# Kernel tuning notes

Hardware: AMD Instinct MI355X
Metric: run time of the kernel (lower is better)

## Reference

```python
import jax, jax.numpy as jnp
import numpy as np

B, S, IN, H, NH = 64, 512, 512, 1024, 4
HD = H // NH
A, HID = 18, 1024
EPS = 1e-5


def _ln(x, w, eps=EPS):
    mu = jnp.mean(x, axis=-1, keepdims=True)
    var = jnp.mean((x - mu) ** 2, axis=-1, keepdims=True)
    return (x - mu) * jax.lax.rsqrt(var + eps) * w


def setup_inputs() -> dict:
    key = jax.random.key(0)
    ks = jax.random.split(key, 12)
    g = lambda k, shape, s: jax.random.normal(k, shape, jnp.float32) * s
    return {
        "obs": g(ks[0], (B, S, IN), 1.0),
        "slstm_state": jnp.zeros((4, B, H), jnp.float32),  # (y, c, n, m)
        "W_in": g(ks[1], (H, IN), IN ** -0.5),
        "b_in": jnp.zeros((H,), jnp.float32),
        "ln1_w": jnp.ones((H,), jnp.float32),
        "w_gates": g(ks[2], (4, NH, HD, HD), HD ** -0.5),  # i,f,z,o headwise input proj
        "R": g(ks[3], (NH, HD, 4, HD), HD ** -0.5),        # headwise recurrent kernel
        "b_gates": jnp.zeros((4, H), jnp.float32),
        "gn_w": jnp.ones((H,), jnp.float32),               # multi-head group norm weight
        "ln_post_w": jnp.ones((H,), jnp.float32),          # post-blocks norm
        "W_hid": g(ks[4], (HID, H), H ** -0.5), "b_hid": jnp.zeros((HID,), jnp.float32),
        "W_pol": g(ks[5], (HID, HID), HID ** -0.5), "b_pol": jnp.zeros((HID,), jnp.float32),
        "W_val": g(ks[6], (HID, HID), HID ** -0.5), "b_val": jnp.zeros((HID,), jnp.float32),
        "W_act": g(ks[7], (A, HID), 0.01), "b_act": jnp.zeros((A,), jnp.float32),
        "W_v": g(ks[8], (1, HID), HID ** -0.5), "b_v": jnp.zeros((1,), jnp.float32),
    }


def reference(obs, slstm_state, W_in, b_in, ln1_w, w_gates, R, b_gates, gn_w,
              ln_post_w, W_hid, b_hid, W_pol, b_pol, W_val, b_val, W_act, b_act, W_v, b_v):
    b, s, _ = obs.shape
    # input projection (input_size != hidden_size -> nn.Linear)
    x_proj = obs @ W_in.T + b_in                      # (B,S,H)
    # sLSTM block pre-norm
    xn = _ln(x_proj, ln1_w)
    xh = xn.reshape(b, s, NH, HD)
    # headwise (block-diagonal) gate input preactivations, time-major for scan
    gx = jnp.einsum('bsnd,gnde->sgbne', xh, w_gates)  # (S,4,B,NH,HD)
    bg = b_gates.reshape(4, 1, NH, HD)
    st = slstm_state.reshape(4, b, NH, HD)

    def step(carry, gx_t):
        h, c, n, m = carry
        raw = gx_t + jnp.einsum('bnd,ndge->gbne', h, R) + bg  # (4,B,NH,HD)
        iraw, fraw, zraw, oraw = raw
        logfplusm = m + jax.nn.log_sigmoid(fraw)
        mnew = jnp.maximum(iraw, logfplusm)
        i = jnp.exp(iraw - mnew)
        f = jnp.exp(logfplusm - mnew)
        cnew = f * c + i * jnp.tanh(zraw)
        nnew = f * n + i
        hnew = jax.nn.sigmoid(oraw) * cnew / nnew
        return (hnew, cnew, nnew, mnew), hnew

    _, ys = jax.lax.scan(step, (st[0], st[1], st[2], st[3]), gx)  # (S,B,NH,HD)
    y = jnp.transpose(ys, (1, 0, 2, 3))               # (B,S,NH,HD)
    # multi-head group norm over head_dim, then residual
    mu = jnp.mean(y, axis=-1, keepdims=True)
    var = jnp.mean((y - mu) ** 2, axis=-1, keepdims=True)
    y_gn = (y - mu) * jax.lax.rsqrt(var + EPS) * gn_w.reshape(NH, HD)
    out = x_proj + y_gn.reshape(b, s, H)
    out = _ln(out, ln_post_w)                         # post_blocks_norm
    # actor-critic heads
    hh = jax.nn.relu(out @ W_hid.T + b_hid)
    hp = jax.nn.relu(hh @ W_pol.T + b_pol)
    hv = jax.nn.relu(hh @ W_val.T + b_val)
    logits = hp @ W_act.T + b_act                     # (B,S,A)
    value = hv @ W_v.T + b_v                          # (B,S,1)
    return logits, value
```

## Files before the change

kernel.cpp:

```cpp
#include <hip/hip_runtime.h>
#include <cstdint>
#include <cstddef>

#define B_ 64
#define S_ 512
#define IN_ 512
#define H_ 1024
#define NH_ 4
#define HD_ 256
#define A_ 18
#define HID_ 1024
#define TCH_ 128
#define NCH_ (S_ / TCH_)

using short8 = __attribute__((ext_vector_type(8))) short;
using f32x4  = __attribute__((ext_vector_type(4))) float;
typedef __attribute__((ext_vector_type(2))) __bf16 bf16x2;

__device__ __forceinline__ unsigned short f2bf(float f) {
  union { float f; unsigned u; } c; c.f = f;
  unsigned r = c.u + 0x7FFFu + ((c.u >> 16) & 1u);
  return (unsigned short)(r >> 16);
}
__device__ __forceinline__ float bf2f(unsigned short h) {
  union { unsigned u; float f; } c; c.u = ((unsigned)h) << 16;
  return c.f;
}
__device__ __forceinline__ unsigned pk2(float a, float b) {
  return (unsigned)f2bf(a) | ((unsigned)f2bf(b) << 16);
}
__device__ __forceinline__ float dot2(unsigned a, unsigned b, float c) {
#if __has_builtin(__builtin_amdgcn_fdot2_f32_bf16)
  return __builtin_amdgcn_fdot2_f32_bf16(__builtin_bit_cast(bf16x2, a),
                                         __builtin_bit_cast(bf16x2, b), c, false);
#else
  float al = __uint_as_float(a << 16), ah = __uint_as_float(a & 0xffff0000u);
  float bl = __uint_as_float(b << 16), bh = __uint_as_float(b & 0xffff0000u);
  return fmaf(ah, bh, fmaf(al, bl, c));
#endif
}

__global__ __launch_bounds__(256) void rtrans_k(const float* __restrict__ R,
                                                unsigned* __restrict__ Rbb,
                                                unsigned* __restrict__ Rl) {
  const int i = blockIdx.x * 256 + threadIdx.x;
  const int dp = i & 127;
  const int e = (i >> 7) & 255;
  const int g = (i >> 15) & 3;
  const int nh = i >> 17;
  const float* rp = R + (((size_t)nh * 256 + 2 * dp) * 4 + g) * 256 + e;
  unsigned lo = f2bf(rp[0]), hi = f2bf(rp[1024]);
  unsigned v = lo | (hi << 16);
  Rbb[i] = v;
  if (dp >= 96) {
    int j = (dp - 96) >> 1, p = (dp - 96) & 1;
    int col = g * 256 + e;
    Rl[((size_t)(j * 4 + nh) * 1024 + col) * 2 + p] = v;
  }
}

__global__ __launch_bounds__(256) void wgt_k(const float* __restrict__ wg,
                                             unsigned short* __restrict__ wgb) {
  const int i = blockIdx.x * 256 + threadIdx.x;
  const int k = i & 255;
  const int e = (i >> 8) & 255;
  const int g = (i >> 16) & 3;
  const int nh = i >> 18;
  wgb[i] = f2bf(wg[(((size_t)(g * 4 + nh) * 256 + k) * 256) + e]);
}

__global__ __launch_bounds__(256) void rowstats_k(const unsigned short* __restrict__ x,
                                                  float* __restrict__ rs) {
  const int r = blockIdx.x, tid = threadIdx.x;
  const int lane = tid & 63, wave = tid >> 6;
  ushort4 u = *(const ushort4*)(x + (size_t)r * H_ + tid * 4);
  float v0 = bf2f(u.x), v1 = bf2f(u.y), v2 = bf2f(u.z), v3 = bf2f(u.w);
  float s1 = v0 + v1 + v2 + v3;
  float s2 = v0 * v0 + v1 * v1 + v2 * v2 + v3 * v3;
#pragma unroll
  for (int off = 32; off; off >>= 1) { s1 += __shfl_xor(s1, off); s2 += __shfl_xor(s2, off); }
  __shared__ float a1[4], a2[4];
  if (lane == 0) { a1[wave] = s1; a2[wave] = s2; }
  __syncthreads();
  if (tid == 0) {
    float S1 = a1[0] + a1[1] + a1[2] + a1[3];
    float S2 = a2[0] + a2[1] + a2[2] + a2[3];
    float mu = S1 * (1.f / H_);
    float var = S2 * (1.f / H_) - mu * mu;
    rs[r * 2] = mu;
    rs[r * 2 + 1] = rsqrtf(var + 1e-5f);
  }
}

template <int AMODE, int BMODE, bool RELU, int OUTMODE>
__global__ __launch_bounds__(256) void mgemm_k(
    const void* __restrict__ Av, const void* __restrict__ Wv,
    const float* __restrict__ bias, const float* __restrict__ rs,
    const float* __restrict__ lnw, unsigned short* __restrict__ Cb,
    int K, int lda, int chunk) {
  __shared__ uint4 As4[4][128];
  __shared__ uint4 Bs4[4][128];
  const int tid = threadIdx.x;
  const int lane = tid & 63, wave = tid >> 6;
  const int wr = wave >> 1, wc = wave & 1;
  const int col0 = blockIdx.y * 128;
  int nh = 0, g = 0, aoff = 0, bb = 0;
  size_t wbase = 0;
  if constexpr (OUTMODE == 1) {
    int z = blockIdx.z; nh = z >> 2; g = z & 3;
    aoff = nh * HD_;
    bb = blockIdx.x;
    wbase = (size_t)(nh * 4 + g) * 256 * 256;
  }
  auto arow = [&](int mm) -> int {
    if constexpr (OUTMODE == 1) return bb * 512 + chunk * TCH_ + mm;
    else return (int)blockIdx.x * 128 + mm;
  };
  f32x4 acc[4][4];
#pragma unroll
  for (int m = 0; m < 4; ++m)
#pragma unroll
    for (int n = 0; n < 4; ++n) acc[m][n] = 0.f;

  const int sm = tid >> 1;
  const int sh = tid & 1;

  for (int k0 = 0; k0 < K; k0 += 32) {
    {
      int rg = arow(sm);
      unsigned pk[8];
      if constexpr (AMODE == 0) {
        const float* ap = (const float*)Av + (size_t)rg * lda + k0 + sh * 16;
#pragma unroll
        for (int q = 0; q < 4; ++q) {
          float4 f = ((const float4*)ap)[q];
          pk[2 * q] = pk2(f.x, f.y); pk[2 * q + 1] = pk2(f.z, f.w);
        }
      } else if constexpr (AMODE == 1) {
        const uint4* ap = (const uint4*)((const unsigned short*)Av + (size_t)rg * lda + aoff + k0 + sh * 16);
        uint4 u0 = ap[0], u1 = ap[1];
        pk[0] = u0.x; pk[1] = u0.y; pk[2] = u0.z; pk[3] = u0.w;
        pk[4] = u1.x; pk[5] = u1.y; pk[6] = u1.z; pk[7] = u1.w;
      } else {
        const uint4* ap = (const uint4*)((const unsigned short*)Av + (size_t)rg * lda + aoff + k0 + sh * 16);
        uint4 u0 = ap[0], u1 = ap[1];
        unsigned w8[8] = {u0.x, u0.y, u0.z, u0.w, u1.x, u1.y, u1.z, u1.w};
        float mu = rs[rg * 2], rstd = rs[rg * 2 + 1];
        const float* lw = lnw + aoff + k0 + sh * 16;
#pragma unroll
        for (int q = 0; q < 8; ++q) {
          float lo = (bf2f((unsigned short)w8[q]) - mu) * rstd * lw[2 * q];
          float hi = (bf2f((unsigned short)(w8[q] >> 16)) - mu) * rstd * lw[2 * q + 1];
          pk[q] = pk2(lo, hi);
        }
      }
      As4[2 * sh][sm]     = uint4{pk[0], pk[1], pk[2], pk[3]};
      As4[2 * sh + 1][sm] = uint4{pk[4], pk[5], pk[6], pk[7]};
    }
    {
      unsigned pk[8];
      if constexpr (BMODE == 0) {
        const float* wp = (const float*)Wv + (size_t)(col0 + sm) * K + k0 + sh * 16;
#pragma unroll
        for (int q = 0; q < 4; ++q) {
          float4 f = ((const float4*)wp)[q];
          pk[2 * q] = pk2(f.x, f.y); pk[2 * q + 1] = pk2(f.z, f.w);
        }
      } else {
        const uint4* wp = (const uint4*)((const unsigned short*)Wv + wbase + (size_t)(col0 + sm) * 256 + k0 + sh * 16);
        uint4 u0 = wp[0], u1 = wp[1];
        pk[0] = u0.x; pk[1] = u0.y; pk[2] = u0.z; pk[3] = u0.w;
        pk[4] = u1.x; pk[5] = u1.y; pk[6] = u1.z; pk[7] = u1.w;
      }
      Bs4[2 * sh][sm]     = uint4{pk[0], pk[1], pk[2], pk[3]};
      Bs4[2 * sh + 1][sm] = uint4{pk[4], pk[5], pk[6], pk[7]};
    }
    __syncthreads();
    short8 af[4], bfv[4];
#pragma unroll
    for (int m = 0; m < 4; ++m)
      af[m] = *(const short8*)&As4[lane >> 4][wr * 64 + m * 16 + (lane & 15)];
#pragma unroll
    for (int n = 0; n < 4; ++n)
      bfv[n] = *(const short8*)&Bs4[lane >> 4][wc * 64 + n * 16 + (lane & 15)];
#pragma unroll
    for (int m = 0; m < 4; ++m)
#pragma unroll
      for (int n = 0; n < 4; ++n)
        acc[m][n] = __builtin_amdgcn_mfma_f32_16x16x32_bf16(af[m], bfv[n], acc[m][n], 0, 0, 0);
    __syncthreads();
  }
  if constexpr (OUTMODE == 0) {
#pragma unroll
    for (int n = 0; n < 4; ++n) {
      int c = col0 + wc * 64 + n * 16 + (lane & 15);
      float bc = bias ? bias[c] : 0.f;
#pragma unroll
      for (int m = 0; m < 4; ++m) {
        int r0 = arow(wr * 64 + m * 16 + ((lane >> 4) << 2));
#pragma unroll
        for (int i = 0; i < 4; ++i) {
          float v = acc[m][n][i] + bc;
          if constexpr (RELU) v = fmaxf(v, 0.f);
          Cb[(size_t)(r0 + i) * 1024 + c] = f2bf(v);
        }
      }
    }
  } else {
#pragma unroll
    for (int n = 0; n < 4; ++n) {
      int e = col0 + wc * 64 + n * 16 + (lane & 15);
#pragma unroll
      for (int m = 0; m < 4; ++m) {
        int sl0 = wr * 64 + m * 16 + ((lane >> 4) << 2);
#pragma unroll
        for (int i = 0; i < 4; ++i) {
          int sl = sl0 + i;
          size_t base = (size_t)(sl * 64 + bb) * 4096 + nh * 1024 + g * 256;
          Cb[base + e] = f2bf(acc[m][n][i]);
        }
      }
    }
  }
}

__global__ __launch_bounds__(1024, 1) void scan_k(
    const unsigned short* __restrict__ gxc, const unsigned* __restrict__ Rbb,
    const unsigned* __restrict__ Rl, const float* __restrict__ bgates,
    float* __restrict__ state, unsigned short* __restrict__ y, int chunk) {
  const int tid = threadIdx.x;
  const int bid = blockIdx.x;
  const int nh = bid >> 6, b = bid & 63;
  __shared__ uint2 Rlds[16][1024];
  __shared__ float rawf[1024];
  __shared__ alignas(16) unsigned short hsu[256];

#pragma unroll
  for (int j = 0; j < 16; ++j) {
    const uint2* src = (const uint2*)Rl + (size_t)(j * 4 + nh) * 1024 + tid;
    Rlds[j][tid] = *src;
  }
  unsigned rcol[96];
  {
    const unsigned* rp = Rbb + ((size_t)nh * 1024 + tid) * 128;
#pragma unroll
    for (int i = 0; i < 96; ++i) rcol[i] = rp[i];
  }
  const float bg = bgates[(tid >> 8) * H_ + nh * HD_ + (tid & 255)];

  const size_t sbase = (size_t)b * H_ + nh * HD_ + tid;
  float c_ = 0.f, n_ = 0.f, m_ = 0.f, hlast = 0.f;
  if (tid < 256) {
    hlast = state[sbase];
    c_ = state[65536 + sbase];
    n_ = state[2 * 65536 + sbase];
    m_ = state[3 * 65536 + sbase];
    hsu[tid] = f2bf(hlast);
  }
  __syncthreads();

  const unsigned short* gp = gxc + ((size_t)b * 4 + nh) * 1024 + tid;
  unsigned short* yp = y + ((size_t)(chunk * TCH_) * 64 + b) * H_ + nh * HD_;

  unsigned short gcur = gp[0];

  for (int t = 0; t < TCH_; ++t) {
    float acc = bf2f(gcur) + bg;
    if (t < TCH_ - 1) gcur = gp[(size_t)(t + 1) * 262144];
    const uint4* h4 = (const uint4*)hsu;
#pragma unroll
    for (int q = 0; q < 24; ++q) {
      uint4 hu = h4[q];
      acc = dot2(rcol[4 * q + 0], hu.x, acc);
      acc = dot2(rcol[4 * q + 1], hu.y, acc);
      acc = dot2(rcol[4 * q + 2], hu.z, acc);
      acc = dot2(rcol[4 * q + 3], hu.w, acc);
    }
#pragma unroll
    for (int s = 0; s < 8; ++s) {
      uint4 hu = h4[24 + s];
      uint2 r0 = Rlds[2 * s][tid];
      uint2 r1 = Rlds[2 * s + 1][tid];
      acc = dot2(r0.x, hu.x, acc);
      acc = dot2(r0.y, hu.y, acc);
      acc = dot2(r1.x, hu.z, acc);
      acc = dot2(r1.y, hu.w, acc);
    }
    rawf[tid] = acc;
    __syncthreads();
    if (tid < 256) {
      float iraw = rawf[tid];
      float fraw = rawf[256 + tid];
      float zraw = rawf[512 + tid];
      float oraw = rawf[768 + tid];
      float ls = -log1pf(expf(-fabsf(fraw)));
      if (fraw < 0.f) ls += fraw;
      float lfm = m_ + ls;
      float mnew = fmaxf(iraw, lfm);
      float iv = expf(iraw - mnew);
      float fv = expf(lfm - mnew);
      c_ = fv * c_ + iv * tanhf(zraw);
      n_ = fv * n_ + iv;
      m_ = mnew;
      hlast = c_ / n_ / (1.f + expf(-oraw));
      unsigned short hb = f2bf(hlast);
      hsu[tid] = hb;
      yp[(size_t)t * 65536 + tid] = hb;
    }
    __syncthreads();
  }
  if (tid < 256) {
    state[sbase] = hlast;
    state[65536 + sbase] = c_;
    state[2 * 65536 + sbase] = n_;
    state[3 * 65536 + sbase] = m_;
  }
}

__global__ __launch_bounds__(256) void post_k(
    const unsigned short* __restrict__ y, const unsigned short* __restrict__ xp,
    const float* __restrict__ gnw, const float* __restrict__ lpw,
    unsigned short* __restrict__ outb) {
  const int r = blockIdx.x;
  const int b = r >> 9, s = r & 511;
  const int tid = threadIdx.x;
  const int lane = tid & 63, wave = tid >> 6;
  ushort4 yu = *(const ushort4*)(y + (size_t)(s * 64 + b) * H_ + tid * 4);
  float v[4] = {bf2f(yu.x), bf2f(yu.y), bf2f(yu.z), bf2f(yu.w)};
  float s1 = v[0] + v[1] + v[2] + v[3];
  float s2 = v[0] * v[0] + v[1] * v[1] + v[2] * v[2] + v[3] * v[3];
#pragma unroll
  for (int off = 32; off; off >>= 1) { s1 += __shfl_xor(s1, off); s2 += __shfl_xor(s2, off); }
  float mu = s1 * (1.f / HD_);
  float rstd = rsqrtf(s2 * (1.f / HD_) - mu * mu + 1e-5f);
  float4 g4 = *(const float4*)(gnw + tid * 4);
  ushort4 xu = *(const ushort4*)(xp + (size_t)r * H_ + tid * 4);
  float o[4];
  o[0] = fmaf((v[0] - mu) * rstd, g4.x, bf2f(xu.x));
  o[1] = fmaf((v[1] - mu) * rstd, g4.y, bf2f(xu.y));
  o[2] = fmaf((v[2] - mu) * rstd, g4.z, bf2f(xu.z));
  o[3] = fmaf((v[3] - mu) * rstd, g4.w, bf2f(xu.w));
  float t1 = o[0] + o[1] + o[2] + o[3];
  float t2 = o[0] * o[0] + o[1] * o[1] + o[2] * o[2] + o[3] * o[3];
#pragma unroll
  for (int off = 32; off; off >>= 1) { t1 += __shfl_xor(t1, off); t2 += __shfl_xor(t2, off); }
  __shared__ float a1[4], a2[4];
  if (lane == 0) { a1[wave] = t1; a2[wave] = t2; }
  __syncthreads();
  float T1 = a1[0] + a1[1] + a1[2] + a1[3];
  float T2 = a2[0] + a2[1] + a2[2] + a2[3];
  float MU = T1 * (1.f / H_);
  float RS = rsqrtf(T2 * (1.f / H_) - MU * MU + 1e-5f);
  float4 w4 = *(const float4*)(lpw + tid * 4);
  ushort4 res = {f2bf((o[0] - MU) * RS * w4.x), f2bf((o[1] - MU) * RS * w4.y),
                 f2bf((o[2] - MU) * RS * w4.z), f2bf((o[3] - MU) * RS * w4.w)};
  *(ushort4*)(outb + (size_t)r * H_ + tid * 4) = res;
}

__global__ __launch_bounds__(256) void heads_k(
    const unsigned short* __restrict__ hp, const unsigned short* __restrict__ hv,
    const float* __restrict__ Wact, const float* __restrict__ bact,
    const float* __restrict__ Wv, const float* __restrict__ bv,
    float* __restrict__ dout) {
  const int lane = threadIdx.x & 63, wave = threadIdx.x >> 6;
  const int r = blockIdx.x * 4 + wave;
  const unsigned short* hpr = hp + (size_t)r * HID_;
  const unsigned short* hvr = hv + (size_t)r * HID_;
  float acc[A_];
#pragma unroll
  for (int j = 0; j < A_; ++j) acc[j] = 0.f;
  float accv = 0.f;
  for (int i = 0; i < 16; ++i) {
    int k = i * 64 + lane;
    float hpv = bf2f(hpr[k]);
    float hvv = bf2f(hvr[k]);
#pragma unroll
    for (int j = 0; j < A_; ++j) acc[j] = fmaf(hpv, Wact[j * HID_ + k], acc[j]);
    accv = fmaf(hvv, Wv[k], accv);
  }
#pragma unroll
  for (int j = 0; j < A_; ++j)
#pragma unroll
    for (int off = 32; off; off >>= 1) acc[j] += __shfl_xor(acc[j], off);
#pragma unroll
  for (int off = 32; off; off >>= 1) accv += __shfl_xor(accv, off);
  if (lane == 0) {
#pragma unroll
    for (int j = 0; j < A_; ++j) dout[(size_t)r * A_ + j] = acc[j] + bact[j];
    dout[589824 + r] = accv + bv[0];
  }
}

extern "C" void kernel_launch(void* const* d_in, const int* in_sizes, int n_in,
                              void* d_out, int out_size, void* d_ws, size_t ws_size,
                              hipStream_t stream) {
  const float* obs   = (const float*)d_in[0];
  const float* st    = (const float*)d_in[1];
  const float* W_in  = (const float*)d_in[2];
  const float* b_in  = (const float*)d_in[3];
  const float* ln1w  = (const float*)d_in[4];
  const float* wg    = (const float*)d_in[5];
  const float* R     = (const float*)d_in[6];
  const float* bgat  = (const float*)d_in[7];
  const float* gnw   = (const float*)d_in[8];
  const float* lpw   = (const float*)d_in[9];
  const float* W_hid = (const float*)d_in[10];
  const float* b_hid = (const float*)d_in[11];
  const float* W_pol = (const float*)d_in[12];
  const float* b_pol = (const float*)d_in[13];
  const float* W_val = (const float*)d_in[14];
  const float* b_val = (const float*)d_in[15];
  const float* W_act = (const float*)d_in[16];
  const float* b_act = (const float*)d_in[17];
  const float* W_v   = (const float*)d_in[18];
  const float* b_v   = (const float*)d_in[19];

  const size_t NEEDED = 207618048;
  if (ws_size < NEEDED) return;
  char* ws = (char*)d_ws;
  unsigned short* xproj = (unsigned short*)(ws + 0);
  unsigned short* gxc   = (unsigned short*)(ws + 67108864);
  unsigned short* ybuf  = (unsigned short*)(ws + 134217728);
  float* statebuf       = (float*)(ws + 201326592);
  float* rstat          = (float*)(ws + 202375168);
  unsigned* Rbb         = (unsigned*)(ws + 202899456);
  unsigned short* wgb   = (unsigned short*)(ws + 204996608);
  unsigned* Rl          = (unsigned*)(ws + 207093760);
  unsigned short* outb  = gxc;
  unsigned short* hh    = xproj;
  unsigned short* hp    = ybuf;
  unsigned short* hv    = gxc;
  float* dout = (float*)d_out;

  hipMemcpyAsync(statebuf, st, 4 * 65536 * sizeof(float), hipMemcpyDeviceToDevice, stream);
  rtrans_k<<<2048, 256, 0, stream>>>(R, Rbb, Rl);
  wgt_k<<<4096, 256, 0, stream>>>(wg, wgb);
  mgemm_k<0, 0, false, 0><<<dim3(256, 8), 256, 0, stream>>>(
      obs, W_in, b_in, nullptr, nullptr, xproj, 512, 512, 0);
  rowstats_k<<<32768, 256, 0, stream>>>(xproj, rstat);
  for (int c = 0; c < NCH_; ++c) {
    mgemm_k<2, 1, false, 1><<<dim3(64, 2, 16), 256, 0, stream>>>(
        xproj, wgb, nullptr, rstat, ln1w, gxc, 256, 1024, c);
    scan_k<<<256, 1024, 0, stream>>>(gxc, Rbb, Rl, bgat, statebuf, ybuf, c);
  }
  post_k<<<32768, 256, 0, stream>>>(ybuf, xproj, gnw, lpw, outb);
  mgemm_k<1, 0, true, 0><<<dim3(256, 8), 256, 0, stream>>>(
      outb, W_hid, b_hid, nullptr, nullptr, hh, 1024, 1024, 0);
  mgemm_k<1, 0, true, 0><<<dim3(256, 8), 256, 0, stream>>>(
      hh, W_pol, b_pol, nullptr, nullptr, hp, 1024, 1024, 0);
  mgemm_k<1, 0, true, 0><<<dim3(256, 8), 256, 0, stream>>>(
      hh, W_val, b_val, nullptr, nullptr, hv, 1024, 1024, 0);
  heads_k<<<8192, 256, 0, stream>>>(hp, hv, W_act, b_act, W_v, b_v, dout);
}
```

Before: 2.232 ms.

## Pre-convert GEMM weights to bf16, spread gate nonlinearities across scan threads, inline-asm dot2

```diff
diff --git a/kernel.cpp b/kernel.cpp
--- a/kernel.cpp
+++ b/kernel.cpp
@@ -15,7 +15,6 @@
 
 using short8 = __attribute__((ext_vector_type(8))) short;
 using f32x4  = __attribute__((ext_vector_type(4))) float;
-typedef __attribute__((ext_vector_type(2))) __bf16 bf16x2;
 
 __device__ __forceinline__ unsigned short f2bf(float f) {
   union { float f; unsigned u; } c; c.f = f;
@@ -30,14 +29,9 @@
   return (unsigned)f2bf(a) | ((unsigned)f2bf(b) << 16);
 }
 __device__ __forceinline__ float dot2(unsigned a, unsigned b, float c) {
-#if __has_builtin(__builtin_amdgcn_fdot2_f32_bf16)
-  return __builtin_amdgcn_fdot2_f32_bf16(__builtin_bit_cast(bf16x2, a),
-                                         __builtin_bit_cast(bf16x2, b), c, false);
-#else
-  float al = __uint_as_float(a << 16), ah = __uint_as_float(a & 0xffff0000u);
-  float bl = __uint_as_float(b << 16), bh = __uint_as_float(b & 0xffff0000u);
-  return fmaf(ah, bh, fmaf(al, bl, c));
-#endif
+  float d;
+  asm("v_dot2_f32_bf16 %0, %1, %2, %3" : "=v"(d) : "v"(a), "v"(b), "v"(c));
+  return d;
 }
 
 __global__ __launch_bounds__(256) void rtrans_k(const float* __restrict__ R,
@@ -67,6 +61,12 @@
   const int g = (i >> 16) & 3;
   const int nh = i >> 18;
   wgb[i] = f2bf(wg[(((size_t)(g * 4 + nh) * 256 + k) * 256) + e]);
+}
+
+__global__ __launch_bounds__(256) void wbf_k(const float* __restrict__ src,
+                                             unsigned short* __restrict__ dst, int n) {
+  int i = blockIdx.x * 256 + threadIdx.x;
+  if (i < n) dst[i] = f2bf(src[i]);
 }
 
 __global__ __launch_bounds__(256) void rowstats_k(const unsigned short* __restrict__ x,
@@ -166,8 +166,13 @@
           float4 f = ((const float4*)wp)[q];
           pk[2 * q] = pk2(f.x, f.y); pk[2 * q + 1] = pk2(f.z, f.w);
         }
+      } else if constexpr (BMODE == 1) {
+        const uint4* wp = (const uint4*)((const unsigned short*)Wv + wbase + (size_t)(col0 + sm) * 256 + k0 + sh * 16);
+        uint4 u0 = wp[0], u1 = wp[1];
+        pk[0] = u0.x; pk[1] = u0.y; pk[2] = u0.z; pk[3] = u0.w;
+        pk[4] = u1.x; pk[5] = u1.y; pk[6] = u1.z; pk[7] = u1.w;
       } else {
-        const uint4* wp = (const uint4*)((const unsigned short*)Wv + wbase + (size_t)(col0 + sm) * 256 + k0 + sh * 16);
+        const uint4* wp = (const uint4*)((const unsigned short*)Wv + (size_t)(col0 + sm) * K + k0 + sh * 16);
         uint4 u0 = wp[0], u1 = wp[1];
         pk[0] = u0.x; pk[1] = u0.y; pk[2] = u0.z; pk[3] = u0.w;
         pk[4] = u1.x; pk[5] = u1.y; pk[6] = u1.z; pk[7] = u1.w;
@@ -231,6 +236,7 @@
   const int tid = threadIdx.x;
   const int bid = blockIdx.x;
   const int nh = bid >> 6, b = bid & 63;
+  const int g = tid >> 8;
   __shared__ uint2 Rlds[16][1024];
   __shared__ float rawf[1024];
   __shared__ alignas(16) unsigned short hsu[256];
@@ -246,7 +252,7 @@
 #pragma unroll
     for (int i = 0; i < 96; ++i) rcol[i] = rp[i];
   }
-  const float bg = bgates[(tid >> 8) * H_ + nh * HD_ + (tid & 255)];
+  const float bg = bgates[g * H_ + nh * HD_ + (tid & 255)];
 
   const size_t sbase = (size_t)b * H_ + nh * HD_ + tid;
   float c_ = 0.f, n_ = 0.f, m_ = 0.f, hlast = 0.f;
@@ -286,23 +292,33 @@
       acc = dot2(r1.x, hu.z, acc);
       acc = dot2(r1.y, hu.w, acc);
     }
-    rawf[tid] = acc;
+    float val;
+    if (g == 0) {
+      val = acc;
+    } else if (g == 1) {
+      float ls = -log1pf(expf(-fabsf(acc)));
+      if (acc < 0.f) ls += acc;
+      val = ls;
+    } else if (g == 2) {
+      val = tanhf(acc);
+    } else {
+      val = 1.f / (1.f + expf(-acc));
+    }
+    rawf[tid] = val;
     __syncthreads();
     if (tid < 256) {
       float iraw = rawf[tid];
-      float fraw = rawf[256 + tid];
-      float zraw = rawf[512 + tid];
-      float oraw = rawf[768 + tid];
-      float ls = -log1pf(expf(-fabsf(fraw)));
-      if (fraw < 0.f) ls += fraw;
+      float ls   = rawf[256 + tid];
+      float tz   = rawf[512 + tid];
+      float sg   = rawf[768 + tid];
       float lfm = m_ + ls;
       float mnew = fmaxf(iraw, lfm);
       float iv = expf(iraw - mnew);
       float fv = expf(lfm - mnew);
-      c_ = fv * c_ + iv * tanhf(zraw);
+      c_ = fv * c_ + iv * tz;
       n_ = fv * n_ + iv;
       m_ = mnew;
-      hlast = c_ / n_ / (1.f + expf(-oraw));
+      hlast = sg * c_ / n_;
       unsigned short hb = f2bf(hlast);
       hsu[tid] = hb;
       yp[(size_t)t * 65536 + tid] = hb;
@@ -415,7 +431,7 @@
   const float* W_v   = (const float*)d_in[18];
   const float* b_v   = (const float*)d_in[19];
 
-  const size_t NEEDED = 207618048;
+  const size_t NEEDED = 214958080;
   if (ws_size < NEEDED) return;
   char* ws = (char*)d_ws;
   unsigned short* xproj = (unsigned short*)(ws + 0);
@@ -426,6 +442,10 @@
   unsigned* Rbb         = (unsigned*)(ws + 202899456);
   unsigned short* wgb   = (unsigned short*)(ws + 204996608);
   unsigned* Rl          = (unsigned*)(ws + 207093760);
+  unsigned short* wib   = (unsigned short*)(ws + 207618048);
+  unsigned short* whb   = (unsigned short*)(ws + 208666624);
+  unsigned short* wpb   = (unsigned short*)(ws + 210763776);
+  unsigned short* wvb   = (unsigned short*)(ws + 212860928);
   unsigned short* outb  = gxc;
   unsigned short* hh    = xproj;
   unsigned short* hp    = ybuf;
@@ -435,8 +455,12 @@
   hipMemcpyAsync(statebuf, st, 4 * 65536 * sizeof(float), hipMemcpyDeviceToDevice, stream);
   rtrans_k<<<2048, 256, 0, stream>>>(R, Rbb, Rl);
   wgt_k<<<4096, 256, 0, stream>>>(wg, wgb);
-  mgemm_k<0, 0, false, 0><<<dim3(256, 8), 256, 0, stream>>>(
-      obs, W_in, b_in, nullptr, nullptr, xproj, 512, 512, 0);
+  wbf_k<<<2048, 256, 0, stream>>>(W_in, wib, 524288);
+  wbf_k<<<4096, 256, 0, stream>>>(W_hid, whb, 1048576);
+  wbf_k<<<4096, 256, 0, stream>>>(W_pol, wpb, 1048576);
+  wbf_k<<<4096, 256, 0, stream>>>(W_val, wvb, 1048576);
+  mgemm_k<0, 2, false, 0><<<dim3(256, 8), 256, 0, stream>>>(
+      obs, wib, b_in, nullptr, nullptr, xproj, 512, 512, 0);
   rowstats_k<<<32768, 256, 0, stream>>>(xproj, rstat);
   for (int c = 0; c < NCH_; ++c) {
     mgemm_k<2, 1, false, 1><<<dim3(64, 2, 16), 256, 0, stream>>>(
@@ -444,11 +468,11 @@
     scan_k<<<256, 1024, 0, stream>>>(gxc, Rbb, Rl, bgat, statebuf, ybuf, c);
   }
   post_k<<<32768, 256, 0, stream>>>(ybuf, xproj, gnw, lpw, outb);
-  mgemm_k<1, 0, true, 0><<<dim3(256, 8), 256, 0, stream>>>(
-      outb, W_hid, b_hid, nullptr, nullptr, hh, 1024, 1024, 0);
-  mgemm_k<1, 0, true, 0><<<dim3(256, 8), 256, 0, stream>>>(
-      hh, W_pol, b_pol, nullptr, nullptr, hp, 1024, 1024, 0);
-  mgemm_k<1, 0, true, 0><<<dim3(256, 8), 256, 0, stream>>>(
-      hh, W_val, b_val, nullptr, nullptr, hv, 1024, 1024, 0);
+  mgemm_k<1, 2, true, 0><<<dim3(256, 8), 256, 0, stream>>>(
+      outb, whb, b_hid, nullptr, nullptr, hh, 1024, 1024, 0);
+  mgemm_k<1, 2, true, 0><<<dim3(256, 8), 256, 0, stream>>>(
+      hh, wpb, b_pol, nullptr, nullptr, hp, 1024, 1024, 0);
+  mgemm_k<1, 2, true, 0><<<dim3(256, 8), 256, 0, stream>>>(
+      hh, wvb, b_val, nullptr, nullptr, hv, 1024, 1024, 0);
   heads_k<<<8192, 256, 0, stream>>>(hp, hv, W_act, b_act, W_v, b_v, dout);
 }
```

New measurement: 2.178 ms. 2.4% less time.
